# Kernel tuning notes

Measured on AMD Instinct MI355X. Metric: run time of the kernel, lower is better.

The kernel has to match this reference:

```python
import jax, jax.numpy as jnp
import numpy as np

NUM_ENVS = 16384
N = 12          # decision vars (4 legs x 3D force)
M_CON = 24      # 4 SOC cones (3 each) + 12-dim hardtanh box
A_MIN, A_MAX = -10.0, 10.0
ALPHA, BETA = 1.0, 1.0


def setup_inputs() -> dict:
    key = jax.random.key(0)
    k1, k2, k3, k4 = jax.random.split(key, 4)
    Mw = jax.random.normal(k1, (NUM_ENVS, N, N), dtype=jnp.float32) / np.sqrt(N)
    # P must be SPD for inv/solve as in the original QP setup
    P = Mw @ jnp.swapaxes(Mw, -1, -2) + jnp.eye(N, dtype=jnp.float32)
    q = jax.random.normal(k2, (NUM_ENVS, N), dtype=jnp.float32)
    H = jax.random.normal(k3, (NUM_ENVS, M_CON, N), dtype=jnp.float32) * 0.5
    b = jax.random.normal(k4, (NUM_ENVS, M_CON), dtype=jnp.float32)
    contact_filter = jnp.ones((NUM_ENVS, M_CON), dtype=jnp.float32)
    return {"P": P, "q": q, "H": H, "b": b, "contact_filter": contact_filter, "iters": 100}


def _project(z, cf):
    # z: [B, m, 1]. Faithful to torch: project_onto_soc's only in-place effect on z
    # is z_part *= (z_part[:, 2:3] > 0); the full cone projection result is
    # discarded (returned but never written back). Then hardtanh box, then contact filter.
    Bsz = z.shape[0]
    soc = z[:, :12].reshape(Bsz, 4, 3)               # 4 cones of dim 3
    soc = soc * (soc[:, :, 2:3] > 0)                 # zero cone block if z-component <= 0
    box = jnp.clip(z[:, 12:24], A_MIN, A_MAX)        # hardtanh
    z = jnp.concatenate([soc.reshape(Bsz, 12, 1), box], axis=1)
    return z * cf


def reference(P, q, H, b, contact_filter, iters):
    m = H.shape[1]
    q_ = q[..., None]                                # [B, n, 1]
    b_ = b[..., None]                                # [B, m, 1]
    cf = contact_filter[..., None]                   # [B, m, 1]
    Ht = jnp.swapaxes(H, -1, -2)
    I = jnp.eye(m, dtype=P.dtype)
    Fm = I - H @ jnp.linalg.inv(P + Ht @ H) @ Ht     # [B, m, m]
    mu = Fm @ (H @ jnp.linalg.solve(P, q_) - b_)     # [B, m, 1]
    A = jnp.concatenate([
        jnp.concatenate([Fm, BETA * Fm], axis=2),
        jnp.concatenate([ALPHA * (I - 2.0 * Fm), I - 2.0 * ALPHA * BETA * Fm], axis=2),
    ], axis=1)                                       # [B, 2m, 2m]
    Bv = jnp.concatenate([BETA * mu, -2.0 * ALPHA * BETA * mu], axis=1)  # [B, 2m, 1]

    def step(lz, _):
        lz = A @ lz + Bv
        lz = jnp.concatenate([lz[:, :m], _project(lz[:, m:], cf)], axis=1)
        return lz, None

    lz0 = jnp.zeros((P.shape[0], 2 * m, 1), dtype=P.dtype)
    lz, _ = jax.lax.scan(step, lz0, None, length=iters)
    x = jnp.linalg.pinv(H) @ (lz[:, m:] - b_)        # [B, n, 1]
    return x, lz
```

## Files before the change

kernel.cpp:

```cpp
#include <hip/hip_runtime.h>

#define EPB 32
#define BLOCK 256
#define HS 292
#define GS 148
#define SS 28

#define WFENCE() __builtin_amdgcn_wave_barrier()

#define DPP_XOR1 0xB1
#define DPP_XOR2 0x4E
#define DPP_HMIR 0x141

__device__ __constant__ const int GMAP[8] = {0, 1, 2, 3, 7, 6, 5, 4};

#define FMA4(acc, f, s)                                         \
  acc = fmaf((f).x, (s).x,                                      \
        fmaf((f).y, (s).y,                                      \
        fmaf((f).z, (s).z,                                      \
        fmaf((f).w, (s).w, (acc)))))

#define VFMA(acc, s, v)                                         \
  { (acc).x = fmaf((s), (v).x, (acc).x);                        \
    (acc).y = fmaf((s), (v).y, (acc).y);                        \
    (acc).z = fmaf((s), (v).z, (acc).z);                        \
    (acc).w = fmaf((s), (v).w, (acc).w); }

struct Row6 { float4 a, b, c, d, e, f; };

template<int CTRL>
__device__ __forceinline__ float dppv(float v) {
  return __int_as_float(__builtin_amdgcn_update_dpp(
      0, __float_as_int(v), CTRL, 0xF, 0xF, true));
}

template<int K>
__device__ __forceinline__ float getel(const float4& a, const float4& b, const float4& c) {
  if constexpr (K == 0) return a.x; else if constexpr (K == 1) return a.y;
  else if constexpr (K == 2) return a.z; else if constexpr (K == 3) return a.w;
  else if constexpr (K == 4) return b.x; else if constexpr (K == 5) return b.y;
  else if constexpr (K == 6) return b.z; else if constexpr (K == 7) return b.w;
  else if constexpr (K == 8) return c.x; else if constexpr (K == 9) return c.y;
  else if constexpr (K == 10) return c.z; else return c.w;
}
template<int K>
__device__ __forceinline__ void setel(float4& a, float4& b, float4& c, float v) {
  if constexpr (K == 0) a.x = v; else if constexpr (K == 1) a.y = v;
  else if constexpr (K == 2) a.z = v; else if constexpr (K == 3) a.w = v;
  else if constexpr (K == 4) b.x = v; else if constexpr (K == 5) b.y = v;
  else if constexpr (K == 6) b.z = v; else if constexpr (K == 7) b.w = v;
  else if constexpr (K == 8) c.x = v; else if constexpr (K == 9) c.y = v;
  else if constexpr (K == 10) c.z = v; else c.w = v;
}

template<int K>
__device__ __forceinline__ void gj_step(float* A, int t) {
  if (t == K || t + 8 == K) {
    float4* r = (float4*)(A + K * 12);
    float4 a = r[0], b = r[1], c = r[2];
    float ip = 1.0f / getel<K>(a, b, c);
    setel<K>(a, b, c, 1.0f);
    a.x *= ip; a.y *= ip; a.z *= ip; a.w *= ip;
    b.x *= ip; b.y *= ip; b.z *= ip; b.w *= ip;
    c.x *= ip; c.y *= ip; c.z *= ip; c.w *= ip;
    r[0] = a; r[1] = b; r[2] = c;
  }
  WFENCE();
  const float4* pr = (const float4*)(A + K * 12);
  float4 p0 = pr[0], p1 = pr[1], p2 = pr[2];
  {
    float4* rr = (float4*)(A + t * 12);
    float4 a = rr[0], b = rr[1], c = rr[2];
    float f = getel<K>(a, b, c);
    if (t == K) f = 0.0f; else setel<K>(a, b, c, 0.0f);
    a.x = fmaf(-f, p0.x, a.x); a.y = fmaf(-f, p0.y, a.y);
    a.z = fmaf(-f, p0.z, a.z); a.w = fmaf(-f, p0.w, a.w);
    b.x = fmaf(-f, p1.x, b.x); b.y = fmaf(-f, p1.y, b.y);
    b.z = fmaf(-f, p1.z, b.z); b.w = fmaf(-f, p1.w, b.w);
    c.x = fmaf(-f, p2.x, c.x); c.y = fmaf(-f, p2.y, c.y);
    c.z = fmaf(-f, p2.z, c.z); c.w = fmaf(-f, p2.w, c.w);
    rr[0] = a; rr[1] = b; rr[2] = c;
  }
  if (t < 4) {
    const int i = t + 8;
    float4* rr = (float4*)(A + i * 12);
    float4 a = rr[0], b = rr[1], c = rr[2];
    float f = getel<K>(a, b, c);
    if (i == K) f = 0.0f; else setel<K>(a, b, c, 0.0f);
    a.x = fmaf(-f, p0.x, a.x); a.y = fmaf(-f, p0.y, a.y);
    a.z = fmaf(-f, p0.z, a.z); a.w = fmaf(-f, p0.w, a.w);
    b.x = fmaf(-f, p1.x, b.x); b.y = fmaf(-f, p1.y, b.y);
    b.z = fmaf(-f, p1.z, b.z); b.w = fmaf(-f, p1.w, b.w);
    c.x = fmaf(-f, p2.x, c.x); c.y = fmaf(-f, p2.y, c.y);
    c.z = fmaf(-f, p2.z, c.z); c.w = fmaf(-f, p2.w, c.w);
    rr[0] = a; rr[1] = b; rr[2] = c;
  }
  WFENCE();
}
template<int K>
__device__ __forceinline__ void gj_all(float* A, int t) {
  gj_step<K>(A, t);
  if constexpr (K < 11) gj_all<K + 1>(A, t);
}

__device__ __forceinline__ float dot12(float4 a0, float4 a1, float4 a2,
                                       const float* p) {
  const float4* p4 = (const float4*)p;
  float4 b0 = p4[0], b1 = p4[1], b2 = p4[2];
  float acc = 0.f;
  FMA4(acc, a0, b0); FMA4(acc, a1, b1); FMA4(acc, a2, b2);
  return acc;
}

__device__ __forceinline__ void build_gram_row(const float* myH, float* gi,
                                               int i, bool addP) {
  float4 a0 = {0,0,0,0}, a1 = {0,0,0,0}, a2 = {0,0,0,0};
#pragma unroll
  for (int k = 0; k < 24; ++k) {
    float coef = myH[k * 12 + i];
    const float4* hk = (const float4*)(myH + k * 12);
    float4 h0 = hk[0], h1 = hk[1], h2 = hk[2];
    VFMA(a0, coef, h0); VFMA(a1, coef, h1); VFMA(a2, coef, h2);
  }
  float4* g = (float4*)(gi + i * 12);
  if (addP) {
    float4 q0 = g[0], q1 = g[1], q2 = g[2];
    a0.x += q0.x; a0.y += q0.y; a0.z += q0.z; a0.w += q0.w;
    a1.x += q1.x; a1.y += q1.y; a1.z += q1.z; a1.w += q1.w;
    a2.x += q2.x; a2.y += q2.y; a2.z += q2.z; a2.w += q2.w;
  }
  g[0] = a0; g[1] = a1; g[2] = a2;
}

template<int S>
__device__ __forceinline__ float pel(const float* myH, int r, int t,
                                     float4 gA, float4 gB, float4 gC) {
  constexpr int g = S / 3, k = S % 3;
  const int j = 3 * (t ^ GMAP[g]) + k;
  float v = dot12(gA, gB, gC, myH + j * 12);
  return ((j == r) ? 1.0f : 0.0f) - v;
}

__device__ __forceinline__ Row6 build_row_perm(const float* myH, const float* gi,
                                               int r, int t) {
  const float4* hr4 = (const float4*)(myH + r * 12);
  float4 h0 = hr4[0], h1 = hr4[1], h2 = hr4[2];
  float4 gA = {0,0,0,0}, gB = {0,0,0,0}, gC = {0,0,0,0};
#define ACC_G(c, coef)                                          \
  { const float4* g4 = (const float4*)(gi + (c) * 12);          \
    float4 r0 = g4[0], r1 = g4[1], r2 = g4[2];                  \
    VFMA(gA, coef, r0); VFMA(gB, coef, r1); VFMA(gC, coef, r2); }
  ACC_G(0, h0.x) ACC_G(1, h0.y) ACC_G(2,  h0.z) ACC_G(3,  h0.w)
  ACC_G(4, h1.x) ACC_G(5, h1.y) ACC_G(6,  h1.z) ACC_G(7,  h1.w)
  ACC_G(8, h2.x) ACC_G(9, h2.y) ACC_G(10, h2.z) ACC_G(11, h2.w)
#undef ACC_G
  Row6 R;
  R.a = make_float4(pel<0>(myH,r,t,gA,gB,gC),  pel<1>(myH,r,t,gA,gB,gC),
                    pel<2>(myH,r,t,gA,gB,gC),  pel<3>(myH,r,t,gA,gB,gC));
  R.b = make_float4(pel<4>(myH,r,t,gA,gB,gC),  pel<5>(myH,r,t,gA,gB,gC),
                    pel<6>(myH,r,t,gA,gB,gC),  pel<7>(myH,r,t,gA,gB,gC));
  R.c = make_float4(pel<8>(myH,r,t,gA,gB,gC),  pel<9>(myH,r,t,gA,gB,gC),
                    pel<10>(myH,r,t,gA,gB,gC), pel<11>(myH,r,t,gA,gB,gC));
  R.d = make_float4(pel<12>(myH,r,t,gA,gB,gC), pel<13>(myH,r,t,gA,gB,gC),
                    pel<14>(myH,r,t,gA,gB,gC), pel<15>(myH,r,t,gA,gB,gC));
  R.e = make_float4(pel<16>(myH,r,t,gA,gB,gC), pel<17>(myH,r,t,gA,gB,gC),
                    pel<18>(myH,r,t,gA,gB,gC), pel<19>(myH,r,t,gA,gB,gC));
  R.f = make_float4(pel<20>(myH,r,t,gA,gB,gC), pel<21>(myH,r,t,gA,gB,gC),
                    pel<22>(myH,r,t,gA,gB,gC), pel<23>(myH,r,t,gA,gB,gC));
  return R;
}

template<int S>
__device__ __forceinline__ float bgat(const float* bB, int t) {
  constexpr int g = S / 3, k = S % 3;
  return bB[3 * (t ^ GMAP[g]) + k];
}

__global__ __attribute__((amdgpu_flat_work_group_size(BLOCK, BLOCK),
                          amdgpu_waves_per_eu(1, 4)))
void pdhg_kernel(const float* __restrict__ P, const float* __restrict__ q,
                 const float* __restrict__ H, const float* __restrict__ b,
                 const float* __restrict__ cf, const int* __restrict__ itp,
                 float* __restrict__ out, int Btot) {
  __shared__ __align__(16) float sH[EPB * HS];
  __shared__ __align__(16) float sGi[EPB * GS];
  __shared__ __align__(16) float sB[EPB * SS];
  __shared__ __align__(16) float sAux[EPB * SS];

  const int tid  = threadIdx.x;
  const int wq   = tid >> 6;
  const int lane = tid & 63;
  const int e    = wq * 8 + (lane >> 3);
  const int t    = lane & 7;
  const int env  = blockIdx.x * EPB + e;
  const int envW0 = blockIdx.x * EPB + wq * 8;
  const int niter = itp[0];
  const int r0w = 3 * t;

  {
    const float4* gH = (const float4*)(H + (size_t)envW0 * 288);
#pragma unroll
    for (int rep = 0; rep < 9; ++rep) {
      int i = lane + rep * 64;
      int ee = i / 72, off = i - ee * 72;
      *(float4*)&sH[(wq * 8 + ee) * HS + off * 4] = gH[i];
    }
    const float4* gP = (const float4*)(P + (size_t)envW0 * 144);
#pragma unroll
    for (int rep = 0; rep < 4; ++rep) {
      int i = lane + rep * 64;
      int ee = i / 36, off = i - ee * 36;
      *(float4*)&sGi[(wq * 8 + ee) * GS + off * 4] = gP[i];
    }
    { int i = lane + 256; if (lane < 32) {
        int ee = i / 36, off = i - ee * 36;
        *(float4*)&sGi[(wq * 8 + ee) * GS + off * 4] = gP[i]; } }
    const float4* gq = (const float4*)(q + (size_t)envW0 * 12);
    if (lane < 24) {
      int ee = lane / 3, off = lane - ee * 3;
      *(float4*)&sAux[(wq * 8 + ee) * SS + off * 4] = gq[lane];
    }
    const float4* gb = (const float4*)(b + (size_t)envW0 * 24);
    if (lane < 48) {
      int ee = lane / 6, off = lane - ee * 6;
      *(float4*)&sB[(wq * 8 + ee) * SS + off * 4] = gb[lane];
    }
  }
  WFENCE();

  const float* myH = &sH[e * HS];
  float* giB = &sGi[e * GS];
  float* auxB = &sAux[e * SS];
  const float* bB = &sB[e * SS];

  build_gram_row(myH, giB, t, true);
  if (t < 4) build_gram_row(myH, giB, t + 8, true);
  WFENCE();
  gj_all<0>(giB, t);

  {
    const float4* gr = (const float4*)(giB + t * 12);
    auxB[12 + t] = dot12(gr[0], gr[1], gr[2], auxB);
    if (t < 4) {
      const float4* gr8 = (const float4*)(giB + (t + 8) * 12);
      auxB[12 + t + 8] = dot12(gr8[0], gr8[1], gr8[2], auxB);
    }
  }
  WFENCE();

  Row6 Pm0 = build_row_perm(myH, giB, r0w + 0, t);
  Row6 Pm1 = build_row_perm(myH, giB, r0w + 1, t);
  Row6 Pm2 = build_row_perm(myH, giB, r0w + 2, t);
  float mu0, mu1, mu2;
  {
    const float4* h0 = (const float4*)(myH + (r0w + 0) * 12);
    const float4* h1 = (const float4*)(myH + (r0w + 1) * 12);
    const float4* h2 = (const float4*)(myH + (r0w + 2) * 12);
    const float* y = auxB + 12;
    float u0 = dot12(h0[0], h0[1], h0[2], y);
    float u1 = dot12(h1[0], h1[1], h1[2], y);
    float u2 = dot12(h2[0], h2[1], h2[2], y);
    float4 bg0 = make_float4(bgat<0>(bB,t),  bgat<1>(bB,t),  bgat<2>(bB,t),  bgat<3>(bB,t));
    float4 bg1 = make_float4(bgat<4>(bB,t),  bgat<5>(bB,t),  bgat<6>(bB,t),  bgat<7>(bB,t));
    float4 bg2 = make_float4(bgat<8>(bB,t),  bgat<9>(bB,t),  bgat<10>(bB,t), bgat<11>(bB,t));
    float4 bg3 = make_float4(bgat<12>(bB,t), bgat<13>(bB,t), bgat<14>(bB,t), bgat<15>(bB,t));
    float4 bg4 = make_float4(bgat<16>(bB,t), bgat<17>(bB,t), bgat<18>(bB,t), bgat<19>(bB,t));
    float4 bg5 = make_float4(bgat<20>(bB,t), bgat<21>(bB,t), bgat<22>(bB,t), bgat<23>(bB,t));
    float d0 = 0.f, d1 = 0.f, d2 = 0.f;
    FMA4(d0, Pm0.a, bg0); FMA4(d1, Pm1.a, bg0); FMA4(d2, Pm2.a, bg0);
    FMA4(d0, Pm0.b, bg1); FMA4(d1, Pm1.b, bg1); FMA4(d2, Pm2.b, bg1);
    FMA4(d0, Pm0.c, bg2); FMA4(d1, Pm1.c, bg2); FMA4(d2, Pm2.c, bg2);
    FMA4(d0, Pm0.d, bg3); FMA4(d1, Pm1.d, bg3); FMA4(d2, Pm2.d, bg3);
    FMA4(d0, Pm0.e, bg4); FMA4(d1, Pm1.e, bg4); FMA4(d2, Pm2.e, bg4);
    FMA4(d0, Pm0.f, bg5); FMA4(d1, Pm1.f, bg5); FMA4(d2, Pm2.f, bg5);
    mu0 = u0 - d0;
    mu1 = u1 - d1;
    mu2 = u2 - d2;
  }
  float cfr0 = cf[(size_t)env * 24 + r0w];
  float cfr1 = cf[(size_t)env * 24 + r0w + 1];
  float cfr2 = cf[(size_t)env * 24 + r0w + 2];

  float l0 = 0.f, l1 = 0.f, l2 = 0.f, z0 = 0.f, z1 = 0.f, z2 = 0.f;
  for (int it = 0; it < niter; ++it) {
    float s0 = l0 + z0, s1 = l1 + z1, s2 = l2 + z2;
    float g3  = dppv<DPP_XOR1>(s0), g4  = dppv<DPP_XOR1>(s1), g5  = dppv<DPP_XOR1>(s2);
    float g6  = dppv<DPP_XOR2>(s0), g7  = dppv<DPP_XOR2>(s1), g8  = dppv<DPP_XOR2>(s2);
    float g9  = dppv<DPP_XOR2>(g3), g10 = dppv<DPP_XOR2>(g4), g11 = dppv<DPP_XOR2>(g5);
    float g12 = dppv<DPP_HMIR>(s0), g13 = dppv<DPP_HMIR>(s1), g14 = dppv<DPP_HMIR>(s2);
    float g15 = dppv<DPP_HMIR>(g3), g16 = dppv<DPP_HMIR>(g4), g17 = dppv<DPP_HMIR>(g5);
    float g18 = dppv<DPP_HMIR>(g6), g19 = dppv<DPP_HMIR>(g7), g20 = dppv<DPP_HMIR>(g8);
    float g21 = dppv<DPP_HMIR>(g9), g22 = dppv<DPP_HMIR>(g10), g23 = dppv<DPP_HMIR>(g11);
    float4 v0 = make_float4(s0,  s1,  s2,  g3);
    float4 v1 = make_float4(g4,  g5,  g6,  g7);
    float4 v2 = make_float4(g8,  g9,  g10, g11);
    float4 v3 = make_float4(g12, g13, g14, g15);
    float4 v4 = make_float4(g16, g17, g18, g19);
    float4 v5 = make_float4(g20, g21, g22, g23);
    float a0 = mu0, a1 = mu1, a2 = mu2, b0 = 0.f, b1 = 0.f, b2 = 0.f;
    FMA4(a0, Pm0.a, v0); FMA4(a1, Pm1.a, v0); FMA4(a2, Pm2.a, v0);
    FMA4(a0, Pm0.b, v1); FMA4(a1, Pm1.b, v1); FMA4(a2, Pm2.b, v1);
    FMA4(a0, Pm0.c, v2); FMA4(a1, Pm1.c, v2); FMA4(a2, Pm2.c, v2);
    FMA4(b0, Pm0.d, v3); FMA4(b1, Pm1.d, v3); FMA4(b2, Pm2.d, v3);
    FMA4(b0, Pm0.e, v4); FMA4(b1, Pm1.e, v4); FMA4(b2, Pm2.e, v4);
    FMA4(b0, Pm0.f, v5); FMA4(b1, Pm1.f, v5); FMA4(b2, Pm2.f, v5);
    float w0 = a0 + b0, w1 = a1 + b1, w2 = a2 + b2;
    float zp0 = fmaf(-2.0f, w0, s0);
    float zp1 = fmaf(-2.0f, w1, s1);
    float zp2 = fmaf(-2.0f, w2, s2);
    l0 = w0; l1 = w1; l2 = w2;
    if (t < 4) {
      float m = (zp2 > 0.0f) ? 1.0f : 0.0f;
      z0 = zp0 * m * cfr0; z1 = zp1 * m * cfr1; z2 = zp2 * m * cfr2;
    } else {
      z0 = fminf(fmaxf(zp0, -10.0f), 10.0f) * cfr0;
      z1 = fminf(fmaxf(zp1, -10.0f), 10.0f) * cfr1;
      z2 = fminf(fmaxf(zp2, -10.0f), 10.0f) * cfr2;
    }
  }

  float* xout  = out;
  float* lzout = out + (size_t)Btot * 12;
  lzout[(size_t)env * 48 + r0w]          = l0;
  lzout[(size_t)env * 48 + r0w + 1]      = l1;
  lzout[(size_t)env * 48 + r0w + 2]      = l2;
  lzout[(size_t)env * 48 + 24 + r0w]     = z0;
  lzout[(size_t)env * 48 + 24 + r0w + 1] = z1;
  lzout[(size_t)env * 48 + 24 + r0w + 2] = z2;

  float bo0 = b[(size_t)env * 24 + r0w];
  float bo1 = b[(size_t)env * 24 + r0w + 1];
  float bo2 = b[(size_t)env * 24 + r0w + 2];
  WFENCE();
  auxB[r0w]     = z0 - bo0;
  auxB[r0w + 1] = z1 - bo1;
  auxB[r0w + 2] = z2 - bo2;
  WFENCE();

  float rv0 = 0.f, rv8 = 0.f;
#pragma unroll
  for (int k = 0; k < 24; ++k) rv0 = fmaf(myH[k * 12 + t], auxB[k], rv0);
  if (t < 4) {
#pragma unroll
    for (int k = 0; k < 24; ++k) rv8 = fmaf(myH[k * 12 + t + 8], auxB[k], rv8);
  }
  build_gram_row(myH, giB, t, false);
  if (t < 4) build_gram_row(myH, giB, t + 8, false);
  WFENCE();
  auxB[t] = rv0;
  if (t < 4) auxB[t + 8] = rv8;
  WFENCE();

  gj_all<0>(giB, t);
  {
    const float4* gr = (const float4*)(giB + t * 12);
    xout[(size_t)env * 12 + t] = dot12(gr[0], gr[1], gr[2], auxB);
    if (t < 4) {
      const float4* gr8 = (const float4*)(giB + (t + 8) * 12);
      xout[(size_t)env * 12 + t + 8] = dot12(gr8[0], gr8[1], gr8[2], auxB);
    }
  }
}

extern "C" void kernel_launch(void* const* d_in, const int* in_sizes, int n_in,
                              void* d_out, int out_size, void* d_ws, size_t ws_size,
                              hipStream_t stream) {
  const float* P  = (const float*)d_in[0];
  const float* q  = (const float*)d_in[1];
  const float* H  = (const float*)d_in[2];
  const float* b  = (const float*)d_in[3];
  const float* cf = (const float*)d_in[4];
  const int*   it = (const int*)d_in[5];
  float* out = (float*)d_out;
  const int B = in_sizes[1] / 12;
  const int grid = B / EPB;
  pdhg_kernel<<<grid, BLOCK, 0, stream>>>(P, q, H, b, cf, it, out, B);
}
```

Measured before the change: 153.3 us.

## Keep Gauss-Jordan rows in registers and restructure setup and projection math

Gauss-Jordan elimination now keeps each lane's matrix rows in registers and publishes only the pivot row through LDS, instead of reading and writing every row in shared memory at each step. The setup that builds the permuted Fm rows is reorganised to compute three W rows once and reuse them, GMAP becomes a constexpr, and the projection is made branchless with fmed3. Other changes: b is read from LDS rather than global memory, the residual dot product is vectorised, and the waves-per-EU hint rises to a minimum of 2. The extra live registers may raise pressure, and the new waves-per-EU minimum could force spills.

```diff
diff --git a/kernel.cpp b/kernel.cpp
--- a/kernel.cpp
+++ b/kernel.cpp
@@ -12,7 +12,7 @@
 #define DPP_XOR2 0x4E
 #define DPP_HMIR 0x141
 
-__device__ __constant__ const int GMAP[8] = {0, 1, 2, 3, 7, 6, 5, 4};
+constexpr int GMAP[8] = {0, 1, 2, 3, 7, 6, 5, 4};
 
 #define FMA4(acc, f, s)                                         \
   acc = fmaf((f).x, (s).x,                                      \
@@ -26,7 +26,7 @@
     (acc).z = fmaf((s), (v).z, (acc).z);                        \
     (acc).w = fmaf((s), (v).w, (acc).w); }
 
-struct Row6 { float4 a, b, c, d, e, f; };
+#define ADD4(A, B) { (A).x += (B).x; (A).y += (B).y; (A).z += (B).z; (A).w += (B).w; }
 
 template<int CTRL>
 __device__ __forceinline__ float dppv(float v) {
@@ -53,54 +53,13 @@
   else if constexpr (K == 10) c.z = v; else c.w = v;
 }
 
-template<int K>
-__device__ __forceinline__ void gj_step(float* A, int t) {
-  if (t == K || t + 8 == K) {
-    float4* r = (float4*)(A + K * 12);
-    float4 a = r[0], b = r[1], c = r[2];
-    float ip = 1.0f / getel<K>(a, b, c);
-    setel<K>(a, b, c, 1.0f);
-    a.x *= ip; a.y *= ip; a.z *= ip; a.w *= ip;
-    b.x *= ip; b.y *= ip; b.z *= ip; b.w *= ip;
-    c.x *= ip; c.y *= ip; c.z *= ip; c.w *= ip;
-    r[0] = a; r[1] = b; r[2] = c;
-  }
-  WFENCE();
-  const float4* pr = (const float4*)(A + K * 12);
-  float4 p0 = pr[0], p1 = pr[1], p2 = pr[2];
-  {
-    float4* rr = (float4*)(A + t * 12);
-    float4 a = rr[0], b = rr[1], c = rr[2];
-    float f = getel<K>(a, b, c);
-    if (t == K) f = 0.0f; else setel<K>(a, b, c, 0.0f);
-    a.x = fmaf(-f, p0.x, a.x); a.y = fmaf(-f, p0.y, a.y);
-    a.z = fmaf(-f, p0.z, a.z); a.w = fmaf(-f, p0.w, a.w);
-    b.x = fmaf(-f, p1.x, b.x); b.y = fmaf(-f, p1.y, b.y);
-    b.z = fmaf(-f, p1.z, b.z); b.w = fmaf(-f, p1.w, b.w);
-    c.x = fmaf(-f, p2.x, c.x); c.y = fmaf(-f, p2.y, c.y);
-    c.z = fmaf(-f, p2.z, c.z); c.w = fmaf(-f, p2.w, c.w);
-    rr[0] = a; rr[1] = b; rr[2] = c;
-  }
-  if (t < 4) {
-    const int i = t + 8;
-    float4* rr = (float4*)(A + i * 12);
-    float4 a = rr[0], b = rr[1], c = rr[2];
-    float f = getel<K>(a, b, c);
-    if (i == K) f = 0.0f; else setel<K>(a, b, c, 0.0f);
-    a.x = fmaf(-f, p0.x, a.x); a.y = fmaf(-f, p0.y, a.y);
-    a.z = fmaf(-f, p0.z, a.z); a.w = fmaf(-f, p0.w, a.w);
-    b.x = fmaf(-f, p1.x, b.x); b.y = fmaf(-f, p1.y, b.y);
-    b.z = fmaf(-f, p1.z, b.z); b.w = fmaf(-f, p1.w, b.w);
-    c.x = fmaf(-f, p2.x, c.x); c.y = fmaf(-f, p2.y, c.y);
-    c.z = fmaf(-f, p2.z, c.z); c.w = fmaf(-f, p2.w, c.w);
-    rr[0] = a; rr[1] = b; rr[2] = c;
-  }
-  WFENCE();
-}
-template<int K>
-__device__ __forceinline__ void gj_all(float* A, int t) {
-  gj_step<K>(A, t);
-  if constexpr (K < 11) gj_all<K + 1>(A, t);
+template<int S>
+__device__ __forceinline__ void putS(float4* m, float v) {
+  constexpr int Q = S >> 2, R = S & 3;
+  if constexpr (R == 0) m[Q].x = v;
+  else if constexpr (R == 1) m[Q].y = v;
+  else if constexpr (R == 2) m[Q].z = v;
+  else m[Q].w = v;
 }
 
 __device__ __forceinline__ float dot12(float4 a0, float4 a1, float4 a2,
@@ -112,62 +71,92 @@
   return acc;
 }
 
-__device__ __forceinline__ void build_gram_row(const float* myH, float* gi,
-                                               int i, bool addP) {
-  float4 a0 = {0,0,0,0}, a1 = {0,0,0,0}, a2 = {0,0,0,0};
+template<int K>
+__device__ __forceinline__ void pivot_pub(float4& a, float4& b, float4& c, float* piv) {
+  float ip = 1.0f / getel<K>(a, b, c);
+  setel<K>(a, b, c, 1.0f);
+  a.x *= ip; a.y *= ip; a.z *= ip; a.w *= ip;
+  b.x *= ip; b.y *= ip; b.z *= ip; b.w *= ip;
+  c.x *= ip; c.y *= ip; c.z *= ip; c.w *= ip;
+  float4* pv = (float4*)piv;
+  pv[0] = a; pv[1] = b; pv[2] = c;
+}
+
+#define ELIM(f, A, B, C)                                              \
+  { (A).x = fmaf(-(f), p0.x, (A).x); (A).y = fmaf(-(f), p0.y, (A).y); \
+    (A).z = fmaf(-(f), p0.z, (A).z); (A).w = fmaf(-(f), p0.w, (A).w); \
+    (B).x = fmaf(-(f), p1.x, (B).x); (B).y = fmaf(-(f), p1.y, (B).y); \
+    (B).z = fmaf(-(f), p1.z, (B).z); (B).w = fmaf(-(f), p1.w, (B).w); \
+    (C).x = fmaf(-(f), p2.x, (C).x); (C).y = fmaf(-(f), p2.y, (C).y); \
+    (C).z = fmaf(-(f), p2.z, (C).z); (C).w = fmaf(-(f), p2.w, (C).w); }
+
+template<int K>
+__device__ __forceinline__ void rgj_step(float4& a0, float4& b0, float4& c0,
+                                         float4& a1, float4& b1, float4& c1,
+                                         float* piv, int t) {
+  if constexpr (K < 8) {
+    if (t == K) pivot_pub<K>(a0, b0, c0, piv);
+  } else {
+    if (t == K - 8) pivot_pub<K>(a1, b1, c1, piv);
+  }
+  WFENCE();
+  const float4* pv = (const float4*)piv;
+  float4 p0 = pv[0], p1 = pv[1], p2 = pv[2];
+  {
+    const bool own = (K < 8) && (t == K);
+    float cur = getel<K>(a0, b0, c0);
+    float f = own ? 0.0f : cur;
+    setel<K>(a0, b0, c0, own ? cur : 0.0f);
+    ELIM(f, a0, b0, c0);
+  }
+  {
+    const bool own = (K >= 8) && (t == K - 8);
+    float cur = getel<K>(a1, b1, c1);
+    float f = own ? 0.0f : cur;
+    setel<K>(a1, b1, c1, own ? cur : 0.0f);
+    ELIM(f, a1, b1, c1);
+  }
+  WFENCE();
+}
+
+template<int K>
+__device__ __forceinline__ void rgj_all(float4& a0, float4& b0, float4& c0,
+                                        float4& a1, float4& b1, float4& c1,
+                                        float* piv, int t) {
+  rgj_step<K>(a0, b0, c0, a1, b1, c1, piv, t);
+  if constexpr (K < 11) rgj_all<K + 1>(a0, b0, c0, a1, b1, c1, piv, t);
+}
+
+__device__ __forceinline__ void gram_rows(const float* myH, int t, int i1,
+    float4& a0, float4& b0, float4& c0, float4& a1, float4& b1, float4& c1) {
+  a0 = make_float4(0.f, 0.f, 0.f, 0.f);
+  b0 = a0; c0 = a0; a1 = a0; b1 = a0; c1 = a0;
 #pragma unroll
   for (int k = 0; k < 24; ++k) {
-    float coef = myH[k * 12 + i];
     const float4* hk = (const float4*)(myH + k * 12);
     float4 h0 = hk[0], h1 = hk[1], h2 = hk[2];
-    VFMA(a0, coef, h0); VFMA(a1, coef, h1); VFMA(a2, coef, h2);
-  }
-  float4* g = (float4*)(gi + i * 12);
-  if (addP) {
-    float4 q0 = g[0], q1 = g[1], q2 = g[2];
-    a0.x += q0.x; a0.y += q0.y; a0.z += q0.z; a0.w += q0.w;
-    a1.x += q1.x; a1.y += q1.y; a1.z += q1.z; a1.w += q1.w;
-    a2.x += q2.x; a2.y += q2.y; a2.z += q2.z; a2.w += q2.w;
-  }
-  g[0] = a0; g[1] = a1; g[2] = a2;
-}
-
-template<int S>
-__device__ __forceinline__ float pel(const float* myH, int r, int t,
-                                     float4 gA, float4 gB, float4 gC) {
-  constexpr int g = S / 3, k = S % 3;
-  const int j = 3 * (t ^ GMAP[g]) + k;
-  float v = dot12(gA, gB, gC, myH + j * 12);
-  return ((j == r) ? 1.0f : 0.0f) - v;
-}
-
-__device__ __forceinline__ Row6 build_row_perm(const float* myH, const float* gi,
-                                               int r, int t) {
-  const float4* hr4 = (const float4*)(myH + r * 12);
-  float4 h0 = hr4[0], h1 = hr4[1], h2 = hr4[2];
-  float4 gA = {0,0,0,0}, gB = {0,0,0,0}, gC = {0,0,0,0};
-#define ACC_G(c, coef)                                          \
-  { const float4* g4 = (const float4*)(gi + (c) * 12);          \
-    float4 r0 = g4[0], r1 = g4[1], r2 = g4[2];                  \
-    VFMA(gA, coef, r0); VFMA(gB, coef, r1); VFMA(gC, coef, r2); }
-  ACC_G(0, h0.x) ACC_G(1, h0.y) ACC_G(2,  h0.z) ACC_G(3,  h0.w)
-  ACC_G(4, h1.x) ACC_G(5, h1.y) ACC_G(6,  h1.z) ACC_G(7,  h1.w)
-  ACC_G(8, h2.x) ACC_G(9, h2.y) ACC_G(10, h2.z) ACC_G(11, h2.w)
-#undef ACC_G
-  Row6 R;
-  R.a = make_float4(pel<0>(myH,r,t,gA,gB,gC),  pel<1>(myH,r,t,gA,gB,gC),
-                    pel<2>(myH,r,t,gA,gB,gC),  pel<3>(myH,r,t,gA,gB,gC));
-  R.b = make_float4(pel<4>(myH,r,t,gA,gB,gC),  pel<5>(myH,r,t,gA,gB,gC),
-                    pel<6>(myH,r,t,gA,gB,gC),  pel<7>(myH,r,t,gA,gB,gC));
-  R.c = make_float4(pel<8>(myH,r,t,gA,gB,gC),  pel<9>(myH,r,t,gA,gB,gC),
-                    pel<10>(myH,r,t,gA,gB,gC), pel<11>(myH,r,t,gA,gB,gC));
-  R.d = make_float4(pel<12>(myH,r,t,gA,gB,gC), pel<13>(myH,r,t,gA,gB,gC),
-                    pel<14>(myH,r,t,gA,gB,gC), pel<15>(myH,r,t,gA,gB,gC));
-  R.e = make_float4(pel<16>(myH,r,t,gA,gB,gC), pel<17>(myH,r,t,gA,gB,gC),
-                    pel<18>(myH,r,t,gA,gB,gC), pel<19>(myH,r,t,gA,gB,gC));
-  R.f = make_float4(pel<20>(myH,r,t,gA,gB,gC), pel<21>(myH,r,t,gA,gB,gC),
-                    pel<22>(myH,r,t,gA,gB,gC), pel<23>(myH,r,t,gA,gB,gC));
-  return R;
+    float f0 = myH[k * 12 + t];
+    float f1 = myH[k * 12 + i1];
+    VFMA(a0, f0, h0); VFMA(b0, f0, h1); VFMA(c0, f0, h2);
+    VFMA(a1, f1, h0); VFMA(b1, f1, h1); VFMA(c1, f1, h2);
+  }
+}
+
+template<int g, int k>
+__device__ __forceinline__ void slot3(const float* myH, int t,
+    const float4* W0, const float4* W1, const float4* W2,
+    float4* P0, float4* P1, float4* P2) {
+  const int c = 3 * (t ^ GMAP[g]) + k;
+  const float4* hc = (const float4*)(myH + c * 12);
+  float4 h0 = hc[0], h1 = hc[1], h2 = hc[2];
+  float d0 = 0.f, d1 = 0.f, d2 = 0.f;
+  FMA4(d0, h0, W0[0]); FMA4(d0, h1, W0[1]); FMA4(d0, h2, W0[2]);
+  FMA4(d1, h0, W1[0]); FMA4(d1, h1, W1[1]); FMA4(d1, h2, W1[2]);
+  FMA4(d2, h0, W2[0]); FMA4(d2, h1, W2[1]); FMA4(d2, h2, W2[2]);
+  constexpr int S = 3 * g + k;
+  putS<S>(P0, ((g == 0 && k == 0) ? 1.0f : 0.0f) - d0);
+  putS<S>(P1, ((g == 0 && k == 1) ? 1.0f : 0.0f) - d1);
+  putS<S>(P2, ((g == 0 && k == 2) ? 1.0f : 0.0f) - d2);
 }
 
 template<int S>
@@ -177,7 +166,7 @@
 }
 
 __global__ __attribute__((amdgpu_flat_work_group_size(BLOCK, BLOCK),
-                          amdgpu_waves_per_eu(1, 4)))
+                          amdgpu_waves_per_eu(2, 4)))
 void pdhg_kernel(const float* __restrict__ P, const float* __restrict__ q,
                  const float* __restrict__ H, const float* __restrict__ b,
                  const float* __restrict__ cf, const int* __restrict__ itp,
@@ -196,6 +185,7 @@
   const int envW0 = blockIdx.x * EPB + wq * 8;
   const int niter = itp[0];
   const int r0w = 3 * t;
+  const int i1 = (t < 4) ? t + 8 : t;
 
   {
     const float4* gH = (const float4*)(H + (size_t)envW0 * 288);
@@ -229,37 +219,77 @@
   WFENCE();
 
   const float* myH = &sH[e * HS];
-  float* giB = &sGi[e * GS];
+  float* giB  = &sGi[e * GS];
   float* auxB = &sAux[e * SS];
-  const float* bB = &sB[e * SS];
-
-  build_gram_row(myH, giB, t, true);
-  if (t < 4) build_gram_row(myH, giB, t + 8, true);
-  WFENCE();
-  gj_all<0>(giB, t);
-
-  {
-    const float4* gr = (const float4*)(giB + t * 12);
-    auxB[12 + t] = dot12(gr[0], gr[1], gr[2], auxB);
+  float* bBm  = &sB[e * SS];
+  const float* bB = bBm;
+
+  float4 g0a, g0b, g0c, g1a, g1b, g1c;
+  gram_rows(myH, t, i1, g0a, g0b, g0c, g1a, g1b, g1c);
+  {
+    const float4* p0 = (const float4*)(giB + t * 12);
+    const float4* p1 = (const float4*)(giB + i1 * 12);
+    float4 q0 = p0[0], q1 = p0[1], q2 = p0[2];
+    float4 r0 = p1[0], r1 = p1[1], r2 = p1[2];
+    ADD4(g0a, q0); ADD4(g0b, q1); ADD4(g0c, q2);
+    ADD4(g1a, r0); ADD4(g1b, r1); ADD4(g1c, r2);
+  }
+  rgj_all<0>(g0a, g0b, g0c, g1a, g1b, g1c, auxB + 12, t);
+
+  {
+    float4* w0 = (float4*)(giB + t * 12);
+    w0[0] = g0a; w0[1] = g0b; w0[2] = g0c;
     if (t < 4) {
-      const float4* gr8 = (const float4*)(giB + (t + 8) * 12);
-      auxB[12 + t + 8] = dot12(gr8[0], gr8[1], gr8[2], auxB);
+      float4* w1 = (float4*)(giB + (t + 8) * 12);
+      w1[0] = g1a; w1[1] = g1b; w1[2] = g1c;
     }
   }
-  WFENCE();
-
-  Row6 Pm0 = build_row_perm(myH, giB, r0w + 0, t);
-  Row6 Pm1 = build_row_perm(myH, giB, r0w + 1, t);
-  Row6 Pm2 = build_row_perm(myH, giB, r0w + 2, t);
+  float y0 = dot12(g0a, g0b, g0c, auxB);
+  float y1 = dot12(g1a, g1b, g1c, auxB);
+  WFENCE();
+  auxB[12 + t] = y0;
+  if (t < 4) auxB[20 + t] = y1;
+  WFENCE();
+
+  float4 hr0[3], hr1[3], hr2[3];
+  { const float4* p = (const float4*)(myH + (r0w + 0) * 12); hr0[0]=p[0]; hr0[1]=p[1]; hr0[2]=p[2]; }
+  { const float4* p = (const float4*)(myH + (r0w + 1) * 12); hr1[0]=p[0]; hr1[1]=p[1]; hr1[2]=p[2]; }
+  { const float4* p = (const float4*)(myH + (r0w + 2) * 12); hr2[0]=p[0]; hr2[1]=p[1]; hr2[2]=p[2]; }
+  float u0, u1, u2;
+  {
+    const float4* y4 = (const float4*)(auxB + 12);
+    float4 ya = y4[0], yb = y4[1], yc = y4[2];
+    u0 = 0.f; FMA4(u0, hr0[0], ya); FMA4(u0, hr0[1], yb); FMA4(u0, hr0[2], yc);
+    u1 = 0.f; FMA4(u1, hr1[0], ya); FMA4(u1, hr1[1], yb); FMA4(u1, hr1[2], yc);
+    u2 = 0.f; FMA4(u2, hr2[0], ya); FMA4(u2, hr2[1], yb); FMA4(u2, hr2[2], yc);
+  }
+
+  float4 W0[3], W1[3], W2[3];
+  W0[0] = make_float4(0.f,0.f,0.f,0.f); W0[1] = W0[0]; W0[2] = W0[0];
+  W1[0] = W0[0]; W1[1] = W0[0]; W1[2] = W0[0];
+  W2[0] = W0[0]; W2[1] = W0[0]; W2[2] = W0[0];
+#define ACC_W(c, EX)                                                   \
+  { const float4* g4 = (const float4*)(giB + (c) * 12);                \
+    float4 r0 = g4[0], r1 = g4[1], r2 = g4[2];                         \
+    float k0 = hr0[(c) >> 2].EX, k1 = hr1[(c) >> 2].EX, k2 = hr2[(c) >> 2].EX; \
+    VFMA(W0[0], k0, r0); VFMA(W0[1], k0, r1); VFMA(W0[2], k0, r2);     \
+    VFMA(W1[0], k1, r0); VFMA(W1[1], k1, r1); VFMA(W1[2], k1, r2);     \
+    VFMA(W2[0], k2, r0); VFMA(W2[1], k2, r1); VFMA(W2[2], k2, r2); }
+  ACC_W(0, x) ACC_W(1, y) ACC_W(2,  z) ACC_W(3,  w)
+  ACC_W(4, x) ACC_W(5, y) ACC_W(6,  z) ACC_W(7,  w)
+  ACC_W(8, x) ACC_W(9, y) ACC_W(10, z) ACC_W(11, w)
+#undef ACC_W
+
+  float4 Pm0[6], Pm1[6], Pm2[6];
+#define SL(g, k) slot3<g, k>(myH, t, W0, W1, W2, Pm0, Pm1, Pm2);
+  SL(0,0) SL(0,1) SL(0,2)  SL(1,0) SL(1,1) SL(1,2)
+  SL(2,0) SL(2,1) SL(2,2)  SL(3,0) SL(3,1) SL(3,2)
+  SL(4,0) SL(4,1) SL(4,2)  SL(5,0) SL(5,1) SL(5,2)
+  SL(6,0) SL(6,1) SL(6,2)  SL(7,0) SL(7,1) SL(7,2)
+#undef SL
+
   float mu0, mu1, mu2;
   {
-    const float4* h0 = (const float4*)(myH + (r0w + 0) * 12);
-    const float4* h1 = (const float4*)(myH + (r0w + 1) * 12);
-    const float4* h2 = (const float4*)(myH + (r0w + 2) * 12);
-    const float* y = auxB + 12;
-    float u0 = dot12(h0[0], h0[1], h0[2], y);
-    float u1 = dot12(h1[0], h1[1], h1[2], y);
-    float u2 = dot12(h2[0], h2[1], h2[2], y);
     float4 bg0 = make_float4(bgat<0>(bB,t),  bgat<1>(bB,t),  bgat<2>(bB,t),  bgat<3>(bB,t));
     float4 bg1 = make_float4(bgat<4>(bB,t),  bgat<5>(bB,t),  bgat<6>(bB,t),  bgat<7>(bB,t));
     float4 bg2 = make_float4(bgat<8>(bB,t),  bgat<9>(bB,t),  bgat<10>(bB,t), bgat<11>(bB,t));
@@ -267,12 +297,12 @@
     float4 bg4 = make_float4(bgat<16>(bB,t), bgat<17>(bB,t), bgat<18>(bB,t), bgat<19>(bB,t));
     float4 bg5 = make_float4(bgat<20>(bB,t), bgat<21>(bB,t), bgat<22>(bB,t), bgat<23>(bB,t));
     float d0 = 0.f, d1 = 0.f, d2 = 0.f;
-    FMA4(d0, Pm0.a, bg0); FMA4(d1, Pm1.a, bg0); FMA4(d2, Pm2.a, bg0);
-    FMA4(d0, Pm0.b, bg1); FMA4(d1, Pm1.b, bg1); FMA4(d2, Pm2.b, bg1);
-    FMA4(d0, Pm0.c, bg2); FMA4(d1, Pm1.c, bg2); FMA4(d2, Pm2.c, bg2);
-    FMA4(d0, Pm0.d, bg3); FMA4(d1, Pm1.d, bg3); FMA4(d2, Pm2.d, bg3);
-    FMA4(d0, Pm0.e, bg4); FMA4(d1, Pm1.e, bg4); FMA4(d2, Pm2.e, bg4);
-    FMA4(d0, Pm0.f, bg5); FMA4(d1, Pm1.f, bg5); FMA4(d2, Pm2.f, bg5);
+    FMA4(d0, Pm0[0], bg0); FMA4(d1, Pm1[0], bg0); FMA4(d2, Pm2[0], bg0);
+    FMA4(d0, Pm0[1], bg1); FMA4(d1, Pm1[1], bg1); FMA4(d2, Pm2[1], bg1);
+    FMA4(d0, Pm0[2], bg2); FMA4(d1, Pm1[2], bg2); FMA4(d2, Pm2[2], bg2);
+    FMA4(d0, Pm0[3], bg3); FMA4(d1, Pm1[3], bg3); FMA4(d2, Pm2[3], bg3);
+    FMA4(d0, Pm0[4], bg4); FMA4(d1, Pm1[4], bg4); FMA4(d2, Pm2[4], bg4);
+    FMA4(d0, Pm0[5], bg5); FMA4(d1, Pm1[5], bg5); FMA4(d2, Pm2[5], bg5);
     mu0 = u0 - d0;
     mu1 = u1 - d1;
     mu2 = u2 - d2;
@@ -281,6 +311,9 @@
   float cfr1 = cf[(size_t)env * 24 + r0w + 1];
   float cfr2 = cf[(size_t)env * 24 + r0w + 2];
 
+  const float plo  = (t < 4) ? -3.0e38f : -10.0f;
+  const float phi  = (t < 4) ?  3.0e38f :  10.0f;
+  const float pthr = (t < 4) ? 0.0f     : -3.0e38f;
   float l0 = 0.f, l1 = 0.f, l2 = 0.f, z0 = 0.f, z1 = 0.f, z2 = 0.f;
   for (int it = 0; it < niter; ++it) {
     float s0 = l0 + z0, s1 = l1 + z1, s2 = l2 + z2;
@@ -298,25 +331,24 @@
     float4 v4 = make_float4(g16, g17, g18, g19);
     float4 v5 = make_float4(g20, g21, g22, g23);
     float a0 = mu0, a1 = mu1, a2 = mu2, b0 = 0.f, b1 = 0.f, b2 = 0.f;
-    FMA4(a0, Pm0.a, v0); FMA4(a1, Pm1.a, v0); FMA4(a2, Pm2.a, v0);
-    FMA4(a0, Pm0.b, v1); FMA4(a1, Pm1.b, v1); FMA4(a2, Pm2.b, v1);
-    FMA4(a0, Pm0.c, v2); FMA4(a1, Pm1.c, v2); FMA4(a2, Pm2.c, v2);
-    FMA4(b0, Pm0.d, v3); FMA4(b1, Pm1.d, v3); FMA4(b2, Pm2.d, v3);
-    FMA4(b0, Pm0.e, v4); FMA4(b1, Pm1.e, v4); FMA4(b2, Pm2.e, v4);
-    FMA4(b0, Pm0.f, v5); FMA4(b1, Pm1.f, v5); FMA4(b2, Pm2.f, v5);
+    FMA4(a0, Pm0[0], v0); FMA4(a1, Pm1[0], v0); FMA4(a2, Pm2[0], v0);
+    FMA4(a0, Pm0[1], v1); FMA4(a1, Pm1[1], v1); FMA4(a2, Pm2[1], v1);
+    FMA4(a0, Pm0[2], v2); FMA4(a1, Pm1[2], v2); FMA4(a2, Pm2[2], v2);
+    FMA4(b0, Pm0[3], v3); FMA4(b1, Pm1[3], v3); FMA4(b2, Pm2[3], v3);
+    FMA4(b0, Pm0[4], v4); FMA4(b1, Pm1[4], v4); FMA4(b2, Pm2[4], v4);
+    FMA4(b0, Pm0[5], v5); FMA4(b1, Pm1[5], v5); FMA4(b2, Pm2[5], v5);
     float w0 = a0 + b0, w1 = a1 + b1, w2 = a2 + b2;
     float zp0 = fmaf(-2.0f, w0, s0);
     float zp1 = fmaf(-2.0f, w1, s1);
     float zp2 = fmaf(-2.0f, w2, s2);
     l0 = w0; l1 = w1; l2 = w2;
-    if (t < 4) {
-      float m = (zp2 > 0.0f) ? 1.0f : 0.0f;
-      z0 = zp0 * m * cfr0; z1 = zp1 * m * cfr1; z2 = zp2 * m * cfr2;
-    } else {
-      z0 = fminf(fmaxf(zp0, -10.0f), 10.0f) * cfr0;
-      z1 = fminf(fmaxf(zp1, -10.0f), 10.0f) * cfr1;
-      z2 = fminf(fmaxf(zp2, -10.0f), 10.0f) * cfr2;
-    }
+    bool gt = zp2 > pthr;
+    float e0 = gt ? cfr0 : 0.0f;
+    float e1 = gt ? cfr1 : 0.0f;
+    float e2 = gt ? cfr2 : 0.0f;
+    z0 = __builtin_amdgcn_fmed3f(zp0, plo, phi) * e0;
+    z1 = __builtin_amdgcn_fmed3f(zp1, plo, phi) * e1;
+    z2 = __builtin_amdgcn_fmed3f(zp2, plo, phi) * e2;
   }
 
   float* xout  = out;
@@ -328,9 +360,9 @@
   lzout[(size_t)env * 48 + 24 + r0w + 1] = z1;
   lzout[(size_t)env * 48 + 24 + r0w + 2] = z2;
 
-  float bo0 = b[(size_t)env * 24 + r0w];
-  float bo1 = b[(size_t)env * 24 + r0w + 1];
-  float bo2 = b[(size_t)env * 24 + r0w + 2];
+  float bo0 = bB[r0w];
+  float bo1 = bB[r0w + 1];
+  float bo2 = bB[r0w + 2];
   WFENCE();
   auxB[r0w]     = z0 - bo0;
   auxB[r0w + 1] = z1 - bo1;
@@ -338,28 +370,30 @@
   WFENCE();
 
   float rv0 = 0.f, rv8 = 0.f;
-#pragma unroll
-  for (int k = 0; k < 24; ++k) rv0 = fmaf(myH[k * 12 + t], auxB[k], rv0);
-  if (t < 4) {
-#pragma unroll
-    for (int k = 0; k < 24; ++k) rv8 = fmaf(myH[k * 12 + t + 8], auxB[k], rv8);
-  }
-  build_gram_row(myH, giB, t, false);
-  if (t < 4) build_gram_row(myH, giB, t + 8, false);
+  {
+    const float4* a4 = (const float4*)auxB;
+    float4 au0 = a4[0], au1 = a4[1], au2 = a4[2], au3 = a4[3], au4 = a4[4], au5 = a4[5];
+#define RVS(k, AV) { rv0 = fmaf(myH[(k) * 12 + t],  (AV), rv0);   \
+                     rv8 = fmaf(myH[(k) * 12 + i1], (AV), rv8); }
+    RVS(0,  au0.x) RVS(1,  au0.y) RVS(2,  au0.z) RVS(3,  au0.w)
+    RVS(4,  au1.x) RVS(5,  au1.y) RVS(6,  au1.z) RVS(7,  au1.w)
+    RVS(8,  au2.x) RVS(9,  au2.y) RVS(10, au2.z) RVS(11, au2.w)
+    RVS(12, au3.x) RVS(13, au3.y) RVS(14, au3.z) RVS(15, au3.w)
+    RVS(16, au4.x) RVS(17, au4.y) RVS(18, au4.z) RVS(19, au4.w)
+    RVS(20, au5.x) RVS(21, au5.y) RVS(22, au5.z) RVS(23, au5.w)
+#undef RVS
+  }
+
+  gram_rows(myH, t, i1, g0a, g0b, g0c, g1a, g1b, g1c);
   WFENCE();
   auxB[t] = rv0;
   if (t < 4) auxB[t + 8] = rv8;
   WFENCE();
-
-  gj_all<0>(giB, t);
-  {
-    const float4* gr = (const float4*)(giB + t * 12);
-    xout[(size_t)env * 12 + t] = dot12(gr[0], gr[1], gr[2], auxB);
-    if (t < 4) {
-      const float4* gr8 = (const float4*)(giB + (t + 8) * 12);
-      xout[(size_t)env * 12 + t + 8] = dot12(gr8[0], gr8[1], gr8[2], auxB);
-    }
-  }
+  rgj_all<0>(g0a, g0b, g0c, g1a, g1b, g1c, bBm, t);
+
+  xout[(size_t)env * 12 + t] = dot12(g0a, g0b, g0c, auxB);
+  if (t < 4)
+    xout[(size_t)env * 12 + t + 8] = dot12(g1a, g1b, g1c, auxB);
 }
 
 extern "C" void kernel_launch(void* const* d_in, const int* in_sizes, int n_in,
```

New measurement: 192.4 us. 1.26x slower.
